# Optimization experiments

Measured on AMD Instinct MI355X. Metric: run time of the kernel, lower is better.

Reference implementation:

```python
import jax, jax.numpy as jnp
import numpy as np

B, S, D = 4, 128, 4096
H, KV, HD = 32, 8, 128
REP = H // KV  # GQA repeat factor = 4


def setup_inputs() -> dict:
    key = jax.random.key(0)
    ks = jax.random.split(key, 10)
    scale = 0.02
    x = jax.random.normal(ks[0], (B, S, D), dtype=jnp.float32)
    # projection weights stored as (in, out) so y = x @ W + b (== torch Linear)
    wq = jax.random.normal(ks[1], (D, H * HD), dtype=jnp.float32) * scale
    bq = jax.random.normal(ks[2], (H * HD,), dtype=jnp.float32) * scale
    wk = jax.random.normal(ks[3], (D, KV * HD), dtype=jnp.float32) * scale
    bk = jax.random.normal(ks[4], (KV * HD,), dtype=jnp.float32) * scale
    wv = jax.random.normal(ks[5], (D, KV * HD), dtype=jnp.float32) * scale
    bv = jax.random.normal(ks[6], (KV * HD,), dtype=jnp.float32) * scale
    wo = jax.random.normal(ks[7], (H * HD, D), dtype=jnp.float32) * scale
    bo = jax.random.normal(ks[8], (D,), dtype=jnp.float32) * scale
    # rotary frequencies: theta=10000, half-dim = HD//2 = 64
    inv_freq = 1.0 / (10000.0 ** (jnp.arange(0, HD, 2, dtype=jnp.float32) / HD))
    t = jnp.arange(S, dtype=jnp.float32)
    angles = jnp.outer(t, inv_freq)  # (S, 64)
    freqs_cos = jnp.cos(angles)
    freqs_sin = jnp.sin(angles)
    # additive causal mask (S, S): 0 on/below diagonal, -inf above
    mask = jnp.where(jnp.tril(jnp.ones((S, S), dtype=bool)), 0.0, -jnp.inf).astype(jnp.float32)
    cache_k = jnp.zeros((B, S, KV, HD), dtype=jnp.float32)
    cache_v = jnp.zeros((B, S, KV, HD), dtype=jnp.float32)
    return {
        "x": x, "start_pos": 0, "freqs_cos": freqs_cos, "freqs_sin": freqs_sin,
        "mask": mask, "cache_k": cache_k, "cache_v": cache_v,
        "wq": wq, "bq": bq, "wk": wk, "bk": bk, "wv": wv, "bv": bv,
        "wo": wo, "bo": bo,
    }


def _rope(t, cos, sin):
    # t: (B, S, h, HD); treat last dim as HD//2 complex pairs (real, imag)
    tr = t.reshape(*t.shape[:-1], HD // 2, 2)
    tre, tim = tr[..., 0], tr[..., 1]
    c = cos[None, :, None, :]  # (1, S, 1, HD//2)
    s = sin[None, :, None, :]
    out_re = tre * c - tim * s
    out_im = tre * s + tim * c
    return jnp.stack([out_re, out_im], axis=-1).reshape(t.shape)


def reference(x, start_pos, freqs_cos, freqs_sin, mask, cache_k, cache_v,
              wq, bq, wk, bk, wv, bv, wo, bo):
    bsz, seq_len, _ = x.shape
    q = (x @ wq + bq).reshape(bsz, seq_len, H, HD)
    k = (x @ wk + bk).reshape(bsz, seq_len, KV, HD)
    v = (x @ wv + bv).reshape(bsz, seq_len, KV, HD)
    q = _rope(q, freqs_cos, freqs_sin)
    k = _rope(k, freqs_cos, freqs_sin)
    # KV-cache append (functional)
    cache_k = cache_k.at[:bsz, start_pos:start_pos + seq_len].set(k)
    cache_v = cache_v.at[:bsz, start_pos:start_pos + seq_len].set(v)
    keys = cache_k[:bsz, :start_pos + seq_len]    # (B, T, KV, HD)
    vals = cache_v[:bsz, :start_pos + seq_len]
    # GQA head expansion (repeat_interleave on head dim)
    keys = jnp.repeat(keys, REP, axis=2)          # (B, T, H, HD)
    vals = jnp.repeat(vals, REP, axis=2)
    scale = 1.0 / jnp.sqrt(jnp.float32(HD))
    scores = jnp.einsum('bqhd,bkhd->bhqk', q, keys) * scale + mask
    attn = jax.nn.softmax(scores, axis=-1)
    out = jnp.einsum('bhqk,bkhd->bqhd', attn, vals).reshape(bsz, seq_len, H * HD)
    return out @ wo + bo
```

## Files before the change

### kernel.cpp

```cpp
#include <hip/hip_runtime.h>
#include <math.h>


#define B_   4
#define S_   128
#define D_   4096
#define H_   32
#define KV_  8
#define HD_  128
#define M_   (B_ * S_)
#define NQKV 6144
#define SCALE_ 0.088388347648318447f

typedef _Float16 half_t;
typedef half_t f16x8 __attribute__((ext_vector_type(8)));
typedef float  f32x4 __attribute__((ext_vector_type(4)));
typedef unsigned short ushort;

__device__ inline void load_lds16(const void* g, void* l) {
    __builtin_amdgcn_global_load_lds((const __attribute__((address_space(1))) void*)g,
                                     (__attribute__((address_space(3))) void*)l,
                                     16, 0, 0);
}

__global__ void convert_f16(const float* __restrict__ in, half_t* __restrict__ out,
                            int total4) {
    int i = blockIdx.x * 256 + threadIdx.x;
    if (i >= total4) return;
    float4 f = ((const float4*)in)[i];
    __align__(8) half_t h4[4] = {(half_t)f.x, (half_t)f.y, (half_t)f.z, (half_t)f.w};
    ((uint2*)out)[i] = *(uint2*)h4;
}

__global__ __launch_bounds__(256)
void transpose_qkv(const float* __restrict__ wq, const float* __restrict__ wk,
                   const float* __restrict__ wv, half_t* __restrict__ Wt) {
    __shared__ float tile[64][65];
    const int t = threadIdx.x;
    const int nt = blockIdx.x, k0 = blockIdx.y * 64;
    const float* src; int Nsrc, nsrc0, ndst0;
    if (nt < 64)      { src = wq; Nsrc = 4096; nsrc0 = nt * 64;        ndst0 = nt * 64; }
    else if (nt < 80) { src = wk; Nsrc = 1024; nsrc0 = (nt - 64) * 64; ndst0 = 4096 + (nt - 64) * 64; }
    else              { src = wv; Nsrc = 1024; nsrc0 = (nt - 80) * 64; ndst0 = 5120 + (nt - 80) * 64; }
#pragma unroll
    for (int p = 0; p < 4; ++p) {
        int idx = t + p * 256;
        int r = idx >> 4, c4 = idx & 15;
        float4 w4 = *(const float4*)&src[(size_t)(k0 + r) * Nsrc + nsrc0 + c4 * 4];
        tile[r][c4 * 4 + 0] = w4.x; tile[r][c4 * 4 + 1] = w4.y;
        tile[r][c4 * 4 + 2] = w4.z; tile[r][c4 * 4 + 3] = w4.w;
    }
    __syncthreads();
    const int n = t >> 2, kq = t & 3;
    __align__(16) half_t hs[16];
#pragma unroll
    for (int i = 0; i < 16; ++i)
        hs[i] = (half_t)tile[kq * 16 + i][n];
    size_t ob = (size_t)(ndst0 + n) * 4096 + k0 + kq * 16;
    *(uint4*)&Wt[ob]     = *(uint4*)&hs[0];
    *(uint4*)&Wt[ob + 8] = *(uint4*)&hs[8];
}

__global__ __launch_bounds__(256, 3)
void gemm_f16(const half_t* __restrict__ A16, const half_t* __restrict__ Bt,
              float* __restrict__ Part, int N, int K, int kslice) {
    __shared__ __align__(16) half_t As[128][64];
    __shared__ __align__(16) half_t Bs[128][64];
    const int tid = threadIdx.x;
    const int m0 = blockIdx.y * 128, n0 = blockIdx.x * 128;
    const int kbase = blockIdx.z * kslice;
    const int lane = tid & 63;
    const int quad = lane >> 4, l16 = lane & 15;
    const int w = tid >> 6;
    const int wm = (w & 1) * 64, wn = (w >> 1) * 64;
    const int tB = tid & 192;

    f32x4 acc[4][4] = {};

    for (int kc = kbase; kc < kbase + kslice; kc += 64) {
#pragma unroll
        for (int p = 0; p < 4; ++p) {
            int tb = p * 256 + tB;
            int task = tb + lane;
            int r = task >> 3;
            int os = (task ^ r) & 7;
            load_lds16(&A16[(size_t)(m0 + r) * K + kc + os * 8], (half_t*)As + tb * 8);
            load_lds16(&Bt [(size_t)(n0 + r) * K + kc + os * 8], (half_t*)Bs + tb * 8);
        }
        __syncthreads();
#pragma unroll
        for (int kk = 0; kk < 2; ++kk) {
            f16x8 af[4], bf[4];
#pragma unroll
            for (int i = 0; i < 4; ++i) {
                int ra = wm + i * 16 + l16;
                int rb = wn + i * 16 + l16;
                int L = kk * 4 + quad;
                af[i] = *(const f16x8*)&As[ra][(L ^ (ra & 7)) * 8];
                bf[i] = *(const f16x8*)&Bs[rb][(L ^ (rb & 7)) * 8];
            }
#pragma unroll
            for (int i = 0; i < 4; ++i)
#pragma unroll
                for (int j = 0; j < 4; ++j)
                    acc[i][j] = __builtin_amdgcn_mfma_f32_16x16x32_f16(af[i], bf[j], acc[i][j], 0, 0, 0);
        }
        __syncthreads();
    }
    float* Cp = Part + (size_t)blockIdx.z * ((size_t)M_ * N);
#pragma unroll
    for (int i = 0; i < 4; ++i)
#pragma unroll
        for (int j = 0; j < 4; ++j) {
            int col = n0 + wn + j * 16 + l16;
            int rowb = m0 + wm + i * 16 + quad * 4;
#pragma unroll
            for (int rg = 0; rg < 4; ++rg)
                Cp[(size_t)(rowb + rg) * N + col] = acc[i][j][rg];
        }
}

__global__ void qkv_reduce_rope(const float* __restrict__ Part, int nz,
                                const float* __restrict__ bq, const float* __restrict__ bk,
                                const float* __restrict__ bv,
                                const float* __restrict__ fc, const float* __restrict__ fs,
                                float* __restrict__ qkv) {
    const int row = blockIdx.y;
    const int col = (blockIdx.x * 256 + threadIdx.x) * 2;
    const size_t off = (size_t)row * NQKV + col;
    float2 s = *(const float2*)&Part[off];
    for (int z = 1; z < nz; ++z) {
        float2 p = *(const float2*)&Part[(size_t)z * (M_ * NQKV) + off];
        s.x += p.x; s.y += p.y;
    }
    float2 bi;
    if (col < 4096)      bi = *(const float2*)&bq[col];
    else if (col < 5120) bi = *(const float2*)&bk[col - 4096];
    else                 bi = *(const float2*)&bv[col - 5120];
    s.x += bi.x; s.y += bi.y;
    if (col < 5120) {
        int d2 = (col >> 1) & 63;
        int i = row & 127;
        float c = fc[i * 64 + d2], sn = fs[i * 64 + d2];
        float re = s.x, im = s.y;
        s.x = re * c - im * sn;
        s.y = re * sn + im * c;
    }
    *(float2*)&qkv[off] = s;
}

__global__ void o_reduce(const float* __restrict__ Part, int nz,
                         const float* __restrict__ bo, float* __restrict__ out) {
    const size_t off = (size_t)(blockIdx.x * 256 + threadIdx.x) * 4;
    float4 s = *(const float4*)&Part[off];
    for (int z = 1; z < nz; ++z) {
        float4 p = *(const float4*)&Part[(size_t)z * (M_ * 4096) + off];
        s.x += p.x; s.y += p.y; s.z += p.z; s.w += p.w;
    }
    float4 b = *(const float4*)&bo[off & 4095];
    s.x += b.x; s.y += b.y; s.z += b.z; s.w += b.w;
    *(float4*)&out[off] = s;
}

__global__ __launch_bounds__(256, 2)
void attn_scores_kernel(const float* __restrict__ qkv, const float* __restrict__ mask,
                        float* __restrict__ P) {
    const int bh = blockIdx.x;
    const int b = bh >> 5, h = bh & 31, kv = h >> 2;
    __shared__ float Qs[16][132];
    __shared__ float Ks[16][132];
    const int tid = threadIdx.x;
    const int tx = tid & 15, ty = tid >> 4;

    float acc[8][8];
#pragma unroll
    for (int i = 0; i < 8; ++i)
#pragma unroll
        for (int j = 0; j < 8; ++j) acc[i][j] = 0.f;

    for (int d0 = 0; d0 < HD_; d0 += 16) {
#pragma unroll
        for (int t = 0; t < 2; ++t) {
            int task = tid + t * 256;
            int rr = task >> 2, c = task & 3;
            int dd = d0 + c * 4;
            float4 a4 = *(const float4*)&qkv[(size_t)(b * S_ + rr) * NQKV + h * 128 + dd];
            Qs[c * 4 + 0][rr] = a4.x; Qs[c * 4 + 1][rr] = a4.y;
            Qs[c * 4 + 2][rr] = a4.z; Qs[c * 4 + 3][rr] = a4.w;
            float4 k4 = *(const float4*)&qkv[(size_t)(b * S_ + rr) * NQKV + 4096 + kv * 128 + dd];
            Ks[c * 4 + 0][rr] = k4.x; Ks[c * 4 + 1][rr] = k4.y;
            Ks[c * 4 + 2][rr] = k4.z; Ks[c * 4 + 3][rr] = k4.w;
        }
        __syncthreads();
#pragma unroll
        for (int kk = 0; kk < 16; ++kk) {
            float a[8], bb[8];
            *(float4*)&a[0]  = *(const float4*)&Qs[kk][ty * 4];
            *(float4*)&a[4]  = *(const float4*)&Qs[kk][64 + ty * 4];
            *(float4*)&bb[0] = *(const float4*)&Ks[kk][tx * 4];
            *(float4*)&bb[4] = *(const float4*)&Ks[kk][64 + tx * 4];
#pragma unroll
            for (int i = 0; i < 8; ++i)
#pragma unroll
                for (int j = 0; j < 8; ++j)
                    acc[i][j] = fmaf(a[i], bb[j], acc[i][j]);
        }
        __syncthreads();
    }
#pragma unroll
    for (int ih = 0; ih < 2; ++ih)
#pragma unroll
        for (int i = 0; i < 4; ++i) {
            int row = ih * 64 + ty * 4 + i;
#pragma unroll
            for (int jh = 0; jh < 2; ++jh) {
                int col = jh * 64 + tx * 4;
                float4 r4;
                r4.x = acc[ih*4+i][jh*4+0] * SCALE_ + mask[row * S_ + col + 0];
                r4.y = acc[ih*4+i][jh*4+1] * SCALE_ + mask[row * S_ + col + 1];
                r4.z = acc[ih*4+i][jh*4+2] * SCALE_ + mask[row * S_ + col + 2];
                r4.w = acc[ih*4+i][jh*4+3] * SCALE_ + mask[row * S_ + col + 3];
                *(float4*)&P[((size_t)bh * S_ + row) * S_ + col] = r4;
            }
        }
}

__global__ void softmax_kernel(float* __restrict__ P, int rows) {
    int rI = blockIdx.x * 4 + (threadIdx.x >> 6);
    if (rI >= rows) return;
    int lane = threadIdx.x & 63;
    float* row = P + (size_t)rI * 128;
    float x0 = row[lane], x1 = row[lane + 64];
    float m = fmaxf(x0, x1);
#pragma unroll
    for (int off = 32; off >= 1; off >>= 1)
        m = fmaxf(m, __shfl_xor(m, off, 64));
    float e0 = expf(x0 - m), e1 = expf(x1 - m);
    float s = e0 + e1;
#pragma unroll
    for (int off = 32; off >= 1; off >>= 1)
        s += __shfl_xor(s, off, 64);
    float inv = 1.0f / s;
    row[lane] = e0 * inv;
    row[lane + 64] = e1 * inv;
}

__global__ __launch_bounds__(256, 2)
void attn_pv_kernel(const float* __restrict__ P, const float* __restrict__ qkv,
                    float* __restrict__ atb) {
    const int bh = blockIdx.x;
    const int b = bh >> 5, h = bh & 31, kv = h >> 2;
    __shared__ float Ps[16][132];
    __shared__ float Vs[16][132];
    const int tid = threadIdx.x;
    const int tx = tid & 15, ty = tid >> 4;

    float acc[8][8];
#pragma unroll
    for (int i = 0; i < 8; ++i)
#pragma unroll
        for (int j = 0; j < 8; ++j) acc[i][j] = 0.f;

    for (int j0 = 0; j0 < S_; j0 += 16) {
#pragma unroll
        for (int t = 0; t < 2; ++t) {
            int task = tid + t * 256;
            int rr = task >> 2, c = task & 3;
            float4 p4 = *(const float4*)&P[((size_t)bh * S_ + rr) * S_ + j0 + c * 4];
            Ps[c * 4 + 0][rr] = p4.x; Ps[c * 4 + 1][rr] = p4.y;
            Ps[c * 4 + 2][rr] = p4.z; Ps[c * 4 + 3][rr] = p4.w;
            int rw = task >> 5, cw = task & 31;
            float4 v4 = *(const float4*)&qkv[(size_t)(b * S_ + j0 + rw) * NQKV + 5120 + kv * 128 + cw * 4];
            *(float4*)&Vs[rw][cw * 4] = v4;
        }
        __syncthreads();
#pragma unroll
        for (int kk = 0; kk < 16; ++kk) {
            float a[8], bb[8];
            *(float4*)&a[0]  = *(const float4*)&Ps[kk][ty * 4];
            *(float4*)&a[4]  = *(const float4*)&Ps[kk][64 + ty * 4];
            *(float4*)&bb[0] = *(const float4*)&Vs[kk][tx * 4];
            *(float4*)&bb[4] = *(const float4*)&Vs[kk][64 + tx * 4];
#pragma unroll
            for (int i = 0; i < 8; ++i)
#pragma unroll
                for (int j = 0; j < 8; ++j)
                    acc[i][j] = fmaf(a[i], bb[j], acc[i][j]);
        }
        __syncthreads();
    }
#pragma unroll
    for (int ih = 0; ih < 2; ++ih)
#pragma unroll
        for (int i = 0; i < 4; ++i) {
            int row = ih * 64 + ty * 4 + i;
#pragma unroll
            for (int jh = 0; jh < 2; ++jh) {
                int col = jh * 64 + tx * 4;
                float4 r4;
                r4.x = acc[ih*4+i][jh*4+0];
                r4.y = acc[ih*4+i][jh*4+1];
                r4.z = acc[ih*4+i][jh*4+2];
                r4.w = acc[ih*4+i][jh*4+3];
                *(float4*)&atb[((size_t)(b * S_ + row)) * 4096 + h * 128 + col] = r4;
            }
        }
}

extern "C" void kernel_launch(void* const* d_in, const int* in_sizes, int n_in,
                              void* d_out, int out_size, void* d_ws, size_t ws_size,
                              hipStream_t stream) {
    const float* x    = (const float*)d_in[0];
    const float* fc   = (const float*)d_in[2];
    const float* fs   = (const float*)d_in[3];
    const float* mask = (const float*)d_in[4];
    const float* wq   = (const float*)d_in[7];
    const float* bq   = (const float*)d_in[8];
    const float* wk   = (const float*)d_in[9];
    const float* bk   = (const float*)d_in[10];
    const float* wv   = (const float*)d_in[11];
    const float* bv   = (const float*)d_in[12];
    const float* wo   = (const float*)d_in[13];
    const float* bo   = (const float*)d_in[14];
    float* out = (float*)d_out;

    float*  ws   = (float*)d_ws;
    float*  qkv  = ws;
    half_t* x16  = (half_t*)(qkv + 3145728);
    half_t* a16  = (half_t*)(qkv + 4194304);
    half_t* Wt   = (half_t*)(qkv + 5242880);
    float*  Part = qkv + 17825792;
    float*  Pb   = Part;
    float*  atb  = Part + 2097152;

    const int z = (ws_size >= (size_t)30408704 * 4) ? 4 : 2;
    const int kslice = 4096 / z;

    transpose_qkv<<<dim3(96, 64), 256, 0, stream>>>(wq, wk, wv, Wt);
    convert_f16<<<2048, 256, 0, stream>>>(x, x16, 524288);
    gemm_f16<<<dim3(48, 4, z), 256, 0, stream>>>(x16, Wt, Part, NQKV, 4096, kslice);
    qkv_reduce_rope<<<dim3(12, 512), 256, 0, stream>>>(Part, z, bq, bk, bv, fc, fs, qkv);

    attn_scores_kernel<<<B_ * H_, 256, 0, stream>>>(qkv, mask, Pb);
    softmax_kernel<<<4096, 256, 0, stream>>>(Pb, B_ * H_ * S_);
    attn_pv_kernel<<<B_ * H_, 256, 0, stream>>>(Pb, qkv, atb);

    transpose_qkv<<<dim3(64, 64), 256, 0, stream>>>(wo, wo, wo, Wt);
    convert_f16<<<2048, 256, 0, stream>>>(atb, a16, 524288);
    gemm_f16<<<dim3(32, 4, z), 256, 0, stream>>>(a16, Wt, Part, 4096, 4096, kslice);
    o_reduce<<<2048, 256, 0, stream>>>(Part, z, bo, out);
}
```

Measured before the change: 334.5 us.

## Fuse attention into one MFMA f16 kernel and emit f16 Q/K/V from RoPE

Replaces the three fp32 attention kernels (scores, softmax, PV) with one fused kernel. It uses f16 MFMA for QK^T and PV, computes the causal mask in-kernel and runs the softmax in LDS, so the score matrix never goes through global memory. The QKV reduce/RoPE kernel now writes f16 Q and K plus a transposed f16 V, and the attention output is written directly as f16, which removes the separate convert pass. The weight transpose uses 128-wide tiles with fewer blocks. The cost is lower attention precision (f16 probabilities) and more LDS per block.

```diff
diff --git a/kernel.cpp b/kernel.cpp
--- a/kernel.cpp
+++ b/kernel.cpp
@@ -15,7 +15,6 @@
 typedef _Float16 half_t;
 typedef half_t f16x8 __attribute__((ext_vector_type(8)));
 typedef float  f32x4 __attribute__((ext_vector_type(4)));
-typedef unsigned short ushort;
 
 __device__ inline void load_lds16(const void* g, void* l) {
     __builtin_amdgcn_global_load_lds((const __attribute__((address_space(1))) void*)g,
@@ -33,32 +32,32 @@
 }
 
 __global__ __launch_bounds__(256)
-void transpose_qkv(const float* __restrict__ wq, const float* __restrict__ wk,
-                   const float* __restrict__ wv, half_t* __restrict__ Wt) {
-    __shared__ float tile[64][65];
+void transpose_wf16(const float* __restrict__ wq, const float* __restrict__ wk,
+                    const float* __restrict__ wv, half_t* __restrict__ Wt) {
+    __shared__ __align__(16) float tile[64][132];
     const int t = threadIdx.x;
     const int nt = blockIdx.x, k0 = blockIdx.y * 64;
     const float* src; int Nsrc, nsrc0, ndst0;
-    if (nt < 64)      { src = wq; Nsrc = 4096; nsrc0 = nt * 64;        ndst0 = nt * 64; }
-    else if (nt < 80) { src = wk; Nsrc = 1024; nsrc0 = (nt - 64) * 64; ndst0 = 4096 + (nt - 64) * 64; }
-    else              { src = wv; Nsrc = 1024; nsrc0 = (nt - 80) * 64; ndst0 = 5120 + (nt - 80) * 64; }
-#pragma unroll
-    for (int p = 0; p < 4; ++p) {
+    if (nt < 32)      { src = wq; Nsrc = 4096; nsrc0 = nt * 128;        ndst0 = nt * 128; }
+    else if (nt < 40) { src = wk; Nsrc = 1024; nsrc0 = (nt - 32) * 128; ndst0 = 4096 + (nt - 32) * 128; }
+    else              { src = wv; Nsrc = 1024; nsrc0 = (nt - 40) * 128; ndst0 = 5120 + (nt - 40) * 128; }
+#pragma unroll
+    for (int p = 0; p < 8; ++p) {
         int idx = t + p * 256;
-        int r = idx >> 4, c4 = idx & 15;
-        float4 w4 = *(const float4*)&src[(size_t)(k0 + r) * Nsrc + nsrc0 + c4 * 4];
-        tile[r][c4 * 4 + 0] = w4.x; tile[r][c4 * 4 + 1] = w4.y;
-        tile[r][c4 * 4 + 2] = w4.z; tile[r][c4 * 4 + 3] = w4.w;
-    }
-    __syncthreads();
-    const int n = t >> 2, kq = t & 3;
-    __align__(16) half_t hs[16];
-#pragma unroll
-    for (int i = 0; i < 16; ++i)
-        hs[i] = (half_t)tile[kq * 16 + i][n];
-    size_t ob = (size_t)(ndst0 + n) * 4096 + k0 + kq * 16;
-    *(uint4*)&Wt[ob]     = *(uint4*)&hs[0];
-    *(uint4*)&Wt[ob + 8] = *(uint4*)&hs[8];
+        int r = idx >> 5, c4 = idx & 31;
+        *(float4*)&tile[r][c4 * 4] =
+            *(const float4*)&src[(size_t)(k0 + r) * Nsrc + nsrc0 + c4 * 4];
+    }
+    __syncthreads();
+    const int n = t >> 1, kh = t & 1;
+    __align__(16) half_t hs[32];
+#pragma unroll
+    for (int i = 0; i < 32; ++i)
+        hs[i] = (half_t)tile[kh * 32 + i][n];
+    size_t ob = (size_t)(ndst0 + n) * 4096 + k0 + kh * 32;
+#pragma unroll
+    for (int u = 0; u < 4; ++u)
+        *(uint4*)&Wt[ob + u * 8] = *(uint4*)&hs[u * 8];
 }
 
 __global__ __launch_bounds__(256, 3)
@@ -124,7 +123,8 @@
                                 const float* __restrict__ bq, const float* __restrict__ bk,
                                 const float* __restrict__ bv,
                                 const float* __restrict__ fc, const float* __restrict__ fs,
-                                float* __restrict__ qkv) {
+                                half_t* __restrict__ q16, half_t* __restrict__ k16,
+                                half_t* __restrict__ vt16) {
     const int row = blockIdx.y;
     const int col = (blockIdx.x * 256 + threadIdx.x) * 2;
     const size_t off = (size_t)row * NQKV + col;
@@ -146,7 +146,135 @@
         s.x = re * c - im * sn;
         s.y = re * sn + im * c;
     }
-    *(float2*)&qkv[off] = s;
+    __align__(4) half_t hh[2] = {(half_t)s.x, (half_t)s.y};
+    if (col < 4096) {
+        *(unsigned int*)&q16[(size_t)row * 4096 + col] = *(unsigned int*)hh;
+    } else if (col < 5120) {
+        *(unsigned int*)&k16[(size_t)row * 1024 + (col - 4096)] = *(unsigned int*)hh;
+    } else {
+        int c = col - 5120;
+        int kv = c >> 7, d = c & 127;
+        int b = row >> 7, i = row & 127;
+        size_t base = ((size_t)(b * 8 + kv) * 128 + d) * 128 + i;
+        vt16[base]       = hh[0];
+        vt16[base + 128] = hh[1];
+    }
+}
+
+__global__ __launch_bounds__(256, 2)
+void fused_attn(const half_t* __restrict__ q16, const half_t* __restrict__ k16,
+                const half_t* __restrict__ vt16, half_t* __restrict__ a16) {
+    __shared__ __align__(16) half_t Qs[32][136];
+    __shared__ __align__(16) half_t Ks[128][136];
+    __shared__ float Ps[32][132];
+    __shared__ float red[32][16];
+
+    const int tid = threadIdx.x;
+    const int qi = blockIdx.x & 3, h = (blockIdx.x >> 2) & 31, b = blockIdx.x >> 7;
+    const int kv = h >> 2;
+    const int qbase = qi * 32;
+    const int lane = tid & 63, w = tid >> 6;
+    const int quad = lane >> 4, l16 = lane & 15;
+    const int m0 = (w & 1) * 16, half64 = (w >> 1) * 64;
+
+#pragma unroll
+    for (int p = 0; p < 2; ++p) {
+        int task = tid + p * 256;
+        int r = task >> 4, c = task & 15;
+        *(uint4*)&Qs[r][c * 8] =
+            *(const uint4*)&q16[((size_t)(b * 128 + qbase + r) * 32 + h) * 128 + c * 8];
+    }
+#pragma unroll
+    for (int p = 0; p < 8; ++p) {
+        int task = tid + p * 256;
+        int r = task >> 4, c = task & 15;
+        *(uint4*)&Ks[r][c * 8] =
+            *(const uint4*)&k16[((size_t)(b * 128 + r) * 8 + kv) * 128 + c * 8];
+    }
+    __syncthreads();
+
+    f32x4 s[4] = {};
+#pragma unroll
+    for (int kc = 0; kc < 4; ++kc) {
+        f16x8 af = *(const f16x8*)&Qs[m0 + l16][kc * 32 + quad * 8];
+#pragma unroll
+        for (int jb = 0; jb < 4; ++jb) {
+            f16x8 bf = *(const f16x8*)&Ks[half64 + jb * 16 + l16][kc * 32 + quad * 8];
+            s[jb] = __builtin_amdgcn_mfma_f32_16x16x32_f16(af, bf, s[jb], 0, 0, 0);
+        }
+    }
+#pragma unroll
+    for (int jb = 0; jb < 4; ++jb) {
+        int j = half64 + jb * 16 + l16;
+#pragma unroll
+        for (int rg = 0; rg < 4; ++rg) {
+            int row = m0 + quad * 4 + rg;
+            Ps[row][j] = (j <= qbase + row) ? s[jb][rg] * SCALE_ : -1e30f;
+        }
+    }
+    __syncthreads();
+
+    const int r = tid >> 3, seg = tid & 7;
+    float mx = -1e30f;
+#pragma unroll
+    for (int i = 0; i < 16; ++i) mx = fmaxf(mx, Ps[r][seg * 16 + i]);
+    red[r][seg] = mx;
+    __syncthreads();
+
+    uint4 vstage[8];
+#pragma unroll
+    for (int p = 0; p < 8; ++p) {
+        int task = tid + p * 256;
+        int rr = task >> 4, c = task & 15;
+        vstage[p] = *(const uint4*)&vt16[((size_t)(b * 8 + kv) * 128 + rr) * 128 + c * 8];
+    }
+    float m = red[r][0];
+#pragma unroll
+    for (int i = 1; i < 8; ++i) m = fmaxf(m, red[r][i]);
+    float sum = 0.f;
+#pragma unroll
+    for (int i = 0; i < 16; ++i) {
+        float e = __expf(Ps[r][seg * 16 + i] - m);
+        Ps[r][seg * 16 + i] = e;
+        sum += e;
+    }
+    red[r][8 + seg] = sum;
+#pragma unroll
+    for (int p = 0; p < 8; ++p) {
+        int task = tid + p * 256;
+        int rr = task >> 4, c = task & 15;
+        *(uint4*)&Ks[rr][c * 8] = vstage[p];
+    }
+    __syncthreads();
+
+    float tot = 0.f;
+#pragma unroll
+    for (int i = 0; i < 8; ++i) tot += red[r][8 + i];
+    float inv = 1.0f / tot;
+#pragma unroll
+    for (int i = 0; i < 16; ++i)
+        Qs[r][seg * 16 + i] = (half_t)(Ps[r][seg * 16 + i] * inv);
+    __syncthreads();
+
+    f32x4 o[4] = {};
+#pragma unroll
+    for (int jc = 0; jc < 4; ++jc) {
+        f16x8 af = *(const f16x8*)&Qs[m0 + l16][jc * 32 + quad * 8];
+#pragma unroll
+        for (int db = 0; db < 4; ++db) {
+            f16x8 bf = *(const f16x8*)&Ks[half64 + db * 16 + l16][jc * 32 + quad * 8];
+            o[db] = __builtin_amdgcn_mfma_f32_16x16x32_f16(af, bf, o[db], 0, 0, 0);
+        }
+    }
+#pragma unroll
+    for (int db = 0; db < 4; ++db) {
+        int d = half64 + db * 16 + l16;
+#pragma unroll
+        for (int rg = 0; rg < 4; ++rg) {
+            int row = m0 + quad * 4 + rg;
+            a16[(size_t)(b * 128 + qbase + row) * 4096 + h * 128 + d] = (half_t)o[db][rg];
+        }
+    }
 }
 
 __global__ void o_reduce(const float* __restrict__ Part, int nz,
@@ -162,158 +290,12 @@
     *(float4*)&out[off] = s;
 }
 
-__global__ __launch_bounds__(256, 2)
-void attn_scores_kernel(const float* __restrict__ qkv, const float* __restrict__ mask,
-                        float* __restrict__ P) {
-    const int bh = blockIdx.x;
-    const int b = bh >> 5, h = bh & 31, kv = h >> 2;
-    __shared__ float Qs[16][132];
-    __shared__ float Ks[16][132];
-    const int tid = threadIdx.x;
-    const int tx = tid & 15, ty = tid >> 4;
-
-    float acc[8][8];
-#pragma unroll
-    for (int i = 0; i < 8; ++i)
-#pragma unroll
-        for (int j = 0; j < 8; ++j) acc[i][j] = 0.f;
-
-    for (int d0 = 0; d0 < HD_; d0 += 16) {
-#pragma unroll
-        for (int t = 0; t < 2; ++t) {
-            int task = tid + t * 256;
-            int rr = task >> 2, c = task & 3;
-            int dd = d0 + c * 4;
-            float4 a4 = *(const float4*)&qkv[(size_t)(b * S_ + rr) * NQKV + h * 128 + dd];
-            Qs[c * 4 + 0][rr] = a4.x; Qs[c * 4 + 1][rr] = a4.y;
-            Qs[c * 4 + 2][rr] = a4.z; Qs[c * 4 + 3][rr] = a4.w;
-            float4 k4 = *(const float4*)&qkv[(size_t)(b * S_ + rr) * NQKV + 4096 + kv * 128 + dd];
-            Ks[c * 4 + 0][rr] = k4.x; Ks[c * 4 + 1][rr] = k4.y;
-            Ks[c * 4 + 2][rr] = k4.z; Ks[c * 4 + 3][rr] = k4.w;
-        }
-        __syncthreads();
-#pragma unroll
-        for (int kk = 0; kk < 16; ++kk) {
-            float a[8], bb[8];
-            *(float4*)&a[0]  = *(const float4*)&Qs[kk][ty * 4];
-            *(float4*)&a[4]  = *(const float4*)&Qs[kk][64 + ty * 4];
-            *(float4*)&bb[0] = *(const float4*)&Ks[kk][tx * 4];
-            *(float4*)&bb[4] = *(const float4*)&Ks[kk][64 + tx * 4];
-#pragma unroll
-            for (int i = 0; i < 8; ++i)
-#pragma unroll
-                for (int j = 0; j < 8; ++j)
-                    acc[i][j] = fmaf(a[i], bb[j], acc[i][j]);
-        }
-        __syncthreads();
-    }
-#pragma unroll
-    for (int ih = 0; ih < 2; ++ih)
-#pragma unroll
-        for (int i = 0; i < 4; ++i) {
-            int row = ih * 64 + ty * 4 + i;
-#pragma unroll
-            for (int jh = 0; jh < 2; ++jh) {
-                int col = jh * 64 + tx * 4;
-                float4 r4;
-                r4.x = acc[ih*4+i][jh*4+0] * SCALE_ + mask[row * S_ + col + 0];
-                r4.y = acc[ih*4+i][jh*4+1] * SCALE_ + mask[row * S_ + col + 1];
-                r4.z = acc[ih*4+i][jh*4+2] * SCALE_ + mask[row * S_ + col + 2];
-                r4.w = acc[ih*4+i][jh*4+3] * SCALE_ + mask[row * S_ + col + 3];
-                *(float4*)&P[((size_t)bh * S_ + row) * S_ + col] = r4;
-            }
-        }
-}
-
-__global__ void softmax_kernel(float* __restrict__ P, int rows) {
-    int rI = blockIdx.x * 4 + (threadIdx.x >> 6);
-    if (rI >= rows) return;
-    int lane = threadIdx.x & 63;
-    float* row = P + (size_t)rI * 128;
-    float x0 = row[lane], x1 = row[lane + 64];
-    float m = fmaxf(x0, x1);
-#pragma unroll
-    for (int off = 32; off >= 1; off >>= 1)
-        m = fmaxf(m, __shfl_xor(m, off, 64));
-    float e0 = expf(x0 - m), e1 = expf(x1 - m);
-    float s = e0 + e1;
-#pragma unroll
-    for (int off = 32; off >= 1; off >>= 1)
-        s += __shfl_xor(s, off, 64);
-    float inv = 1.0f / s;
-    row[lane] = e0 * inv;
-    row[lane + 64] = e1 * inv;
-}
-
-__global__ __launch_bounds__(256, 2)
-void attn_pv_kernel(const float* __restrict__ P, const float* __restrict__ qkv,
-                    float* __restrict__ atb) {
-    const int bh = blockIdx.x;
-    const int b = bh >> 5, h = bh & 31, kv = h >> 2;
-    __shared__ float Ps[16][132];
-    __shared__ float Vs[16][132];
-    const int tid = threadIdx.x;
-    const int tx = tid & 15, ty = tid >> 4;
-
-    float acc[8][8];
-#pragma unroll
-    for (int i = 0; i < 8; ++i)
-#pragma unroll
-        for (int j = 0; j < 8; ++j) acc[i][j] = 0.f;
-
-    for (int j0 = 0; j0 < S_; j0 += 16) {
-#pragma unroll
-        for (int t = 0; t < 2; ++t) {
-            int task = tid + t * 256;
-            int rr = task >> 2, c = task & 3;
-            float4 p4 = *(const float4*)&P[((size_t)bh * S_ + rr) * S_ + j0 + c * 4];
-            Ps[c * 4 + 0][rr] = p4.x; Ps[c * 4 + 1][rr] = p4.y;
-            Ps[c * 4 + 2][rr] = p4.z; Ps[c * 4 + 3][rr] = p4.w;
-            int rw = task >> 5, cw = task & 31;
-            float4 v4 = *(const float4*)&qkv[(size_t)(b * S_ + j0 + rw) * NQKV + 5120 + kv * 128 + cw * 4];
-            *(float4*)&Vs[rw][cw * 4] = v4;
-        }
-        __syncthreads();
-#pragma unroll
-        for (int kk = 0; kk < 16; ++kk) {
-            float a[8], bb[8];
-            *(float4*)&a[0]  = *(const float4*)&Ps[kk][ty * 4];
-            *(float4*)&a[4]  = *(const float4*)&Ps[kk][64 + ty * 4];
-            *(float4*)&bb[0] = *(const float4*)&Vs[kk][tx * 4];
-            *(float4*)&bb[4] = *(const float4*)&Vs[kk][64 + tx * 4];
-#pragma unroll
-            for (int i = 0; i < 8; ++i)
-#pragma unroll
-                for (int j = 0; j < 8; ++j)
-                    acc[i][j] = fmaf(a[i], bb[j], acc[i][j]);
-        }
-        __syncthreads();
-    }
-#pragma unroll
-    for (int ih = 0; ih < 2; ++ih)
-#pragma unroll
-        for (int i = 0; i < 4; ++i) {
-            int row = ih * 64 + ty * 4 + i;
-#pragma unroll
-            for (int jh = 0; jh < 2; ++jh) {
-                int col = jh * 64 + tx * 4;
-                float4 r4;
-                r4.x = acc[ih*4+i][jh*4+0];
-                r4.y = acc[ih*4+i][jh*4+1];
-                r4.z = acc[ih*4+i][jh*4+2];
-                r4.w = acc[ih*4+i][jh*4+3];
-                *(float4*)&atb[((size_t)(b * S_ + row)) * 4096 + h * 128 + col] = r4;
-            }
-        }
-}
-
 extern "C" void kernel_launch(void* const* d_in, const int* in_sizes, int n_in,
                               void* d_out, int out_size, void* d_ws, size_t ws_size,
                               hipStream_t stream) {
     const float* x    = (const float*)d_in[0];
     const float* fc   = (const float*)d_in[2];
     const float* fs   = (const float*)d_in[3];
-    const float* mask = (const float*)d_in[4];
     const float* wq   = (const float*)d_in[7];
     const float* bq   = (const float*)d_in[8];
     const float* wk   = (const float*)d_in[9];
@@ -324,29 +306,25 @@
     const float* bo   = (const float*)d_in[14];
     float* out = (float*)d_out;
 
-    float*  ws   = (float*)d_ws;
-    float*  qkv  = ws;
-    half_t* x16  = (half_t*)(qkv + 3145728);
-    half_t* a16  = (half_t*)(qkv + 4194304);
-    half_t* Wt   = (half_t*)(qkv + 5242880);
-    float*  Part = qkv + 17825792;
-    float*  Pb   = Part;
-    float*  atb  = Part + 2097152;
-
-    const int z = (ws_size >= (size_t)30408704 * 4) ? 4 : 2;
+    half_t* x16  = (half_t*)d_ws;
+    half_t* a16  = x16 + 2097152;
+    half_t* q16  = a16 + 2097152;
+    half_t* k16  = q16 + 2097152;
+    half_t* vt16 = k16 + 524288;
+    half_t* Wt   = vt16 + 524288;
+    float*  Part = (float*)(Wt + 25165824);
+
+    const int z = (ws_size >= (size_t)65011712 + (size_t)4 * 12582912) ? 4 : 2;
     const int kslice = 4096 / z;
 
-    transpose_qkv<<<dim3(96, 64), 256, 0, stream>>>(wq, wk, wv, Wt);
+    transpose_wf16<<<dim3(48, 64), 256, 0, stream>>>(wq, wk, wv, Wt);
     convert_f16<<<2048, 256, 0, stream>>>(x, x16, 524288);
     gemm_f16<<<dim3(48, 4, z), 256, 0, stream>>>(x16, Wt, Part, NQKV, 4096, kslice);
-    qkv_reduce_rope<<<dim3(12, 512), 256, 0, stream>>>(Part, z, bq, bk, bv, fc, fs, qkv);
-
-    attn_scores_kernel<<<B_ * H_, 256, 0, stream>>>(qkv, mask, Pb);
-    softmax_kernel<<<4096, 256, 0, stream>>>(Pb, B_ * H_ * S_);
-    attn_pv_kernel<<<B_ * H_, 256, 0, stream>>>(Pb, qkv, atb);
-
-    transpose_qkv<<<dim3(64, 64), 256, 0, stream>>>(wo, wo, wo, Wt);
-    convert_f16<<<2048, 256, 0, stream>>>(atb, a16, 524288);
+    qkv_reduce_rope<<<dim3(12, 512), 256, 0, stream>>>(Part, z, bq, bk, bv, fc, fs,
+                                                       q16, k16, vt16);
+    fused_attn<<<512, 256, 0, stream>>>(q16, k16, vt16, a16);
+
+    transpose_wf16<<<dim3(32, 64), 256, 0, stream>>>(wo, wo, wo, Wt);
     gemm_f16<<<dim3(32, 4, z), 256, 0, stream>>>(a16, Wt, Part, 4096, 4096, kslice);
     o_reduce<<<2048, 256, 0, stream>>>(Part, z, bo, out);
 }
```

After: 303.9 us. 1.1x faster.
